# Performance work log

Hardware: AMD Instinct MI355X
Metric: run time of the kernel (lower is better)

## Reference

```python
import jax, jax.numpy as jnp
import numpy as np

B, S, D_MODEL = 2, 4096, 2048
N_IDX_HEADS, D_HEAD = 4, 64


def setup_inputs() -> dict:
    key = jax.random.key(0)
    k1, k2, k3 = jax.random.split(key, 3)
    h = jax.random.normal(k1, (B, S, D_MODEL), dtype=jnp.float32)
    # torch Linear weights: [out_features, in_features]
    Wq = jax.random.normal(k2, (N_IDX_HEADS * D_HEAD, D_MODEL), dtype=jnp.float32) * (D_MODEL ** -0.5)
    Wk = jax.random.normal(k3, (D_HEAD, D_MODEL), dtype=jnp.float32) * (D_MODEL ** -0.5)
    w = jnp.ones((N_IDX_HEADS,), dtype=jnp.float32)
    return {"h": h, "Wq": Wq, "Wk": Wk, "w": w}


def reference(h, Wq, Wk, w):
    batch, seq, _ = h.shape
    # q: [B, T, H, Dh]; k: [B, S, Dh]
    q = (h @ Wq.T).reshape(batch, seq, N_IDX_HEADS, D_HEAD)
    k = h @ Wk.T
    # scores: [B, T, H, S]
    scores = jax.nn.relu(jnp.einsum('bthd,bsd->bths', q, k))
    # head-weighted sum -> I: [B, T, S]
    I = jnp.einsum('bths,h->bts', scores, w)
    return I
```

## Files before the change

kernel.cpp:

```cpp
#include <hip/hip_runtime.h>

typedef __attribute__((ext_vector_type(8))) short bf16x8;
typedef __attribute__((ext_vector_type(4))) float f32x4;
typedef __attribute__((ext_vector_type(8))) unsigned short us8;

#define K_DIM 2048
#define QK_N  320
#define SEQ   4096
#define BK    64
#define NCHUNK 32
#define NHALF  160
#define BCHUNK 20480

__device__ __forceinline__ unsigned short f2bf(float f) {
    unsigned int u = __builtin_bit_cast(unsigned int, f);
    u += 0x7FFFu + ((u >> 16) & 1u);
    return (unsigned short)(u >> 16);
}

__global__ void cvt_w_swz(const float* __restrict__ Wq,
                          const float* __restrict__ Wk,
                          unsigned short* __restrict__ ws) {
    int id = blockIdx.x * 256 + threadIdx.x;
    int c  = id >> 8;
    int k8 = id & 255;
    int k0 = k8 * 8;
    const float* src = (c < 256) ? (Wq + (size_t)c * K_DIM + k0)
                                 : (Wk + (size_t)(c - 256) * K_DIM + k0);
    float4 v0 = *reinterpret_cast<const float4*>(src);
    float4 v1 = *reinterpret_cast<const float4*>(src + 4);
    us8 o;
    o[0] = f2bf(v0.x); o[1] = f2bf(v0.y); o[2] = f2bf(v0.z); o[3] = f2bf(v0.w);
    o[4] = f2bf(v1.x); o[5] = f2bf(v1.y); o[6] = f2bf(v1.z); o[7] = f2bf(v1.w);
    int half = (c >= NHALF) ? 1 : 0;
    int cc   = c - half * NHALF;
    int kc = k0 / BK;
    int u  = (k0 % BK) >> 3;
    size_t byteoff = (size_t)half * (NCHUNK * (size_t)BCHUNK)
                   + (size_t)kc * BCHUNK + ((size_t)(u * NHALF + cc) * 16);
    *reinterpret_cast<us8*>((char*)ws + byteoff) = o;
}

__global__ __launch_bounds__(256) void proj_gemm(
    const float* __restrict__ A,
    const unsigned short* __restrict__ Wsz,
    unsigned short* __restrict__ C)
{
    const int tid  = threadIdx.x;
    const int lane = tid & 63;
    const int wid  = tid >> 6;
    const int rg   = wid >> 1;
    const int cg   = wid & 1;
    const int half = blockIdx.x;
    const int row0 = blockIdx.y * 32 + rg * 16;
    const int lr = lane & 15, lg = lane >> 4;

    const float* ap = A + (size_t)(row0 + lr) * K_DIM + lg * 8;
    const char* wbase = (const char*)Wsz + (size_t)half * (NCHUNK * (size_t)BCHUNK)
                      + ((cg * 80 + lr) << 4);

    f32x4 acc[5];
#pragma unroll
    for (int j = 0; j < 5; ++j) acc[j] = (f32x4)0.f;

#pragma unroll 2
    for (int t = 0; t < 64; ++t) {
        const char* bu = wbase + (size_t)(t >> 1) * BCHUNK
                       + (size_t)(((t & 1) * 4 + lg) * NHALF) * 16;
        bf16x8 b0 = *reinterpret_cast<const bf16x8*>(bu);
        bf16x8 b1 = *reinterpret_cast<const bf16x8*>(bu + 256);
        bf16x8 b2 = *reinterpret_cast<const bf16x8*>(bu + 512);
        bf16x8 b3 = *reinterpret_cast<const bf16x8*>(bu + 768);
        bf16x8 b4 = *reinterpret_cast<const bf16x8*>(bu + 1024);
        const float* p = ap + t * 32;
        float4 x = *reinterpret_cast<const float4*>(p);
        float4 y = *reinterpret_cast<const float4*>(p + 4);
        bf16x8 a;
        a[0] = (short)f2bf(x.x); a[1] = (short)f2bf(x.y);
        a[2] = (short)f2bf(x.z); a[3] = (short)f2bf(x.w);
        a[4] = (short)f2bf(y.x); a[5] = (short)f2bf(y.y);
        a[6] = (short)f2bf(y.z); a[7] = (short)f2bf(y.w);
        acc[0] = __builtin_amdgcn_mfma_f32_16x16x32_bf16(a, b0, acc[0], 0, 0, 0);
        acc[1] = __builtin_amdgcn_mfma_f32_16x16x32_bf16(a, b1, acc[1], 0, 0, 0);
        acc[2] = __builtin_amdgcn_mfma_f32_16x16x32_bf16(a, b2, acc[2], 0, 0, 0);
        acc[3] = __builtin_amdgcn_mfma_f32_16x16x32_bf16(a, b3, acc[3], 0, 0, 0);
        acc[4] = __builtin_amdgcn_mfma_f32_16x16x32_bf16(a, b4, acc[4], 0, 0, 0);
    }

    const int crow = row0 + lg * 4;
    const int ccol = half * NHALF + cg * 80 + lr;
#pragma unroll
    for (int j = 0; j < 5; ++j)
#pragma unroll
        for (int r = 0; r < 4; ++r)
            C[(size_t)(crow + r) * QK_N + ccol + j * 16] = f2bf(acc[j][r]);
}

__global__ __launch_bounds__(256) void scores_kernel(
    const unsigned short* __restrict__ QK,
    const float* __restrict__ w,
    float* __restrict__ out)
{
    const int lane = threadIdx.x & 63;
    const int wid  = threadIdx.x >> 6;
    const int b  = blockIdx.z;
    const int t0 = blockIdx.y * 128 + (wid >> 1) * 64;
    const int s0 = blockIdx.x * 128 + (wid & 1) * 64;

    const int lr = lane & 15;
    const int lk = (lane >> 4) * 8;
    const int lg = lane >> 4;

    const unsigned short* Qb = QK + (size_t)b * SEQ * QK_N;
    const unsigned short* Kb = Qb + 256;

    float wv[4] = { w[0], w[1], w[2], w[3] };

    f32x4 fin[4][4];
#pragma unroll
    for (int i = 0; i < 4; ++i)
#pragma unroll
        for (int j = 0; j < 4; ++j) fin[i][j] = (f32x4)0.f;

    const unsigned short* qp = Qb + (size_t)(t0 + lr) * QK_N + lk;
    const unsigned short* kp = Kb + (size_t)(s0 + lr) * QK_N + lk;

#pragma unroll
    for (int h = 0; h < 4; ++h) {
        f32x4 acc[4][4];
#pragma unroll
        for (int i = 0; i < 4; ++i)
#pragma unroll
            for (int j = 0; j < 4; ++j) acc[i][j] = (f32x4)0.f;

#pragma unroll
        for (int ks = 0; ks < 2; ++ks) {
            bf16x8 qf[4], kf[4];
#pragma unroll
            for (int i = 0; i < 4; ++i)
                qf[i] = *reinterpret_cast<const bf16x8*>(
                    qp + (size_t)i * 16 * QK_N + h * 64 + ks * 32);
#pragma unroll
            for (int j = 0; j < 4; ++j)
                kf[j] = *reinterpret_cast<const bf16x8*>(
                    kp + (size_t)j * 16 * QK_N + ks * 32);
#pragma unroll
            for (int i = 0; i < 4; ++i)
#pragma unroll
                for (int j = 0; j < 4; ++j)
                    acc[i][j] = __builtin_amdgcn_mfma_f32_16x16x32_bf16(kf[j], qf[i], acc[i][j], 0, 0, 0);
        }
#pragma unroll
        for (int i = 0; i < 4; ++i)
#pragma unroll
            for (int j = 0; j < 4; ++j)
#pragma unroll
                for (int r = 0; r < 4; ++r)
                    fin[i][j][r] += wv[h] * fmaxf(acc[i][j][r], 0.f);
    }

    float* ob = out + (size_t)b * SEQ * SEQ;
#pragma unroll
    for (int i = 0; i < 4; ++i) {
        const size_t rbase = (size_t)(t0 + i * 16 + lr) * SEQ + s0 + lg * 4;
#pragma unroll
        for (int j = 0; j < 4; ++j) {
            float4 v;
            v.x = fin[i][j][0]; v.y = fin[i][j][1];
            v.z = fin[i][j][2]; v.w = fin[i][j][3];
            *reinterpret_cast<float4*>(&ob[rbase + j * 16]) = v;
        }
    }
}

extern "C" void kernel_launch(void* const* d_in, const int* in_sizes, int n_in,
                              void* d_out, int out_size, void* d_ws, size_t ws_size,
                              hipStream_t stream) {
    const float* h  = (const float*)d_in[0];
    const float* Wq = (const float*)d_in[1];
    const float* Wk = (const float*)d_in[2];
    const float* w  = (const float*)d_in[3];
    float* out = (float*)d_out;

    unsigned short* W_swz = (unsigned short*)d_ws;
    unsigned short* QKb   = (unsigned short*)((char*)d_ws + 2 * (size_t)NCHUNK * BCHUNK);

    cvt_w_swz<<<320, 256, 0, stream>>>(Wq, Wk, W_swz);
    proj_gemm<<<dim3(2, 256), 256, 0, stream>>>(h, W_swz, QKb);
    scores_kernel<<<dim3(32, 32, 2), 256, 0, stream>>>(QKb, w, out);
}
```

Measured before the change: 124.3 us.

## Split-K projection GEMM with fp32 partials, reduce kernel, and software-pipelined loads

Splits the K dimension of the projection GEMM into two segments, which doubles the number of blocks (2x256x2) so more of the GPU is filled. Each segment writes fp32 partial results to workspace, and a new reduce kernel sums them and converts to bf16. The inner loop is also rewritten with explicit double-buffered register prefetching of the A and B fragments, and launch bounds now request 4 blocks per CU. The cost is extra fp32 partial-buffer traffic (about 21 MB written and read back) plus one more kernel launch.

```diff
diff --git a/kernel.cpp b/kernel.cpp
--- a/kernel.cpp
+++ b/kernel.cpp
@@ -3,6 +3,7 @@
 typedef __attribute__((ext_vector_type(8))) short bf16x8;
 typedef __attribute__((ext_vector_type(4))) float f32x4;
 typedef __attribute__((ext_vector_type(8))) unsigned short us8;
+typedef __attribute__((ext_vector_type(4))) unsigned short us4;
 
 #define K_DIM 2048
 #define QK_N  320
@@ -11,6 +12,9 @@
 #define NCHUNK 32
 #define NHALF  160
 #define BCHUNK 20480
+#define KSPLIT 2
+#define SEGCHUNK (NCHUNK / KSPLIT)
+#define CPART_ELEMS ((size_t)8192 * QK_N)
 
 __device__ __forceinline__ unsigned short f2bf(float f) {
     unsigned int u = __builtin_bit_cast(unsigned int, f);
@@ -41,10 +45,10 @@
     *reinterpret_cast<us8*>((char*)ws + byteoff) = o;
 }
 
-__global__ __launch_bounds__(256) void proj_gemm(
+__global__ __launch_bounds__(256, 4) void proj_gemm(
     const float* __restrict__ A,
     const unsigned short* __restrict__ Wsz,
-    unsigned short* __restrict__ C)
+    float* __restrict__ Cpart)
 {
     const int tid  = threadIdx.x;
     const int lane = tid & 63;
@@ -52,48 +56,84 @@
     const int rg   = wid >> 1;
     const int cg   = wid & 1;
     const int half = blockIdx.x;
+    const int kseg = blockIdx.z;
     const int row0 = blockIdx.y * 32 + rg * 16;
     const int lr = lane & 15, lg = lane >> 4;
 
-    const float* ap = A + (size_t)(row0 + lr) * K_DIM + lg * 8;
+    const float* ap = A + (size_t)(row0 + lr) * K_DIM + kseg * (K_DIM / KSPLIT) + lg * 8;
     const char* wbase = (const char*)Wsz + (size_t)half * (NCHUNK * (size_t)BCHUNK)
+                      + (size_t)(kseg * SEGCHUNK) * BCHUNK
                       + ((cg * 80 + lr) << 4);
 
     f32x4 acc[5];
 #pragma unroll
     for (int j = 0; j < 5; ++j) acc[j] = (f32x4)0.f;
 
-#pragma unroll 2
-    for (int t = 0; t < 64; ++t) {
-        const char* bu = wbase + (size_t)(t >> 1) * BCHUNK
-                       + (size_t)(((t & 1) * 4 + lg) * NHALF) * 16;
-        bf16x8 b0 = *reinterpret_cast<const bf16x8*>(bu);
-        bf16x8 b1 = *reinterpret_cast<const bf16x8*>(bu + 256);
-        bf16x8 b2 = *reinterpret_cast<const bf16x8*>(bu + 512);
-        bf16x8 b3 = *reinterpret_cast<const bf16x8*>(bu + 768);
-        bf16x8 b4 = *reinterpret_cast<const bf16x8*>(bu + 1024);
-        const float* p = ap + t * 32;
-        float4 x = *reinterpret_cast<const float4*>(p);
-        float4 y = *reinterpret_cast<const float4*>(p + 4);
-        bf16x8 a;
-        a[0] = (short)f2bf(x.x); a[1] = (short)f2bf(x.y);
-        a[2] = (short)f2bf(x.z); a[3] = (short)f2bf(x.w);
-        a[4] = (short)f2bf(y.x); a[5] = (short)f2bf(y.y);
-        a[6] = (short)f2bf(y.z); a[7] = (short)f2bf(y.w);
-        acc[0] = __builtin_amdgcn_mfma_f32_16x16x32_bf16(a, b0, acc[0], 0, 0, 0);
-        acc[1] = __builtin_amdgcn_mfma_f32_16x16x32_bf16(a, b1, acc[1], 0, 0, 0);
-        acc[2] = __builtin_amdgcn_mfma_f32_16x16x32_bf16(a, b2, acc[2], 0, 0, 0);
-        acc[3] = __builtin_amdgcn_mfma_f32_16x16x32_bf16(a, b3, acc[3], 0, 0, 0);
-        acc[4] = __builtin_amdgcn_mfma_f32_16x16x32_bf16(a, b4, acc[4], 0, 0, 0);
+#define LOADB(t, b0, b1, b2, b3, b4) do {                                   \
+        const char* bu = wbase + (size_t)((t) >> 1) * BCHUNK                \
+                       + (size_t)((((t) & 1) * 4 + lg) * NHALF) * 16;       \
+        b0 = *reinterpret_cast<const bf16x8*>(bu);                          \
+        b1 = *reinterpret_cast<const bf16x8*>(bu + 256);                    \
+        b2 = *reinterpret_cast<const bf16x8*>(bu + 512);                    \
+        b3 = *reinterpret_cast<const bf16x8*>(bu + 768);                    \
+        b4 = *reinterpret_cast<const bf16x8*>(bu + 1024);                   \
+    } while (0)
+#define LOADA(t, vx, vy) do {                                               \
+        const float* p = ap + (t) * 32;                                     \
+        vx = *reinterpret_cast<const float4*>(p);                           \
+        vy = *reinterpret_cast<const float4*>(p + 4);                       \
+    } while (0)
+#define COMPUTE(vx, vy, b0, b1, b2, b3, b4) do {                            \
+        bf16x8 a_;                                                          \
+        a_[0] = (short)f2bf(vx.x); a_[1] = (short)f2bf(vx.y);               \
+        a_[2] = (short)f2bf(vx.z); a_[3] = (short)f2bf(vx.w);               \
+        a_[4] = (short)f2bf(vy.x); a_[5] = (short)f2bf(vy.y);               \
+        a_[6] = (short)f2bf(vy.z); a_[7] = (short)f2bf(vy.w);               \
+        acc[0] = __builtin_amdgcn_mfma_f32_16x16x32_bf16(a_, b0, acc[0], 0, 0, 0); \
+        acc[1] = __builtin_amdgcn_mfma_f32_16x16x32_bf16(a_, b1, acc[1], 0, 0, 0); \
+        acc[2] = __builtin_amdgcn_mfma_f32_16x16x32_bf16(a_, b2, acc[2], 0, 0, 0); \
+        acc[3] = __builtin_amdgcn_mfma_f32_16x16x32_bf16(a_, b3, acc[3], 0, 0, 0); \
+        acc[4] = __builtin_amdgcn_mfma_f32_16x16x32_bf16(a_, b4, acc[4], 0, 0, 0); \
+    } while (0)
+
+    bf16x8 cb0, cb1, cb2, cb3, cb4;  float4 cvx, cvy;
+    bf16x8 nb0, nb1, nb2, nb3, nb4;  float4 nvx, nvy;
+
+    LOADB(0, cb0, cb1, cb2, cb3, cb4);
+    LOADA(0, cvx, cvy);
+
+    for (int t = 0; t < 32; t += 2) {
+        LOADB(t + 1, nb0, nb1, nb2, nb3, nb4);
+        LOADA(t + 1, nvx, nvy);
+        COMPUTE(cvx, cvy, cb0, cb1, cb2, cb3, cb4);
+        const int t2 = (t + 2 < 32) ? t + 2 : 31;
+        LOADB(t2, cb0, cb1, cb2, cb3, cb4);
+        LOADA(t2, cvx, cvy);
+        COMPUTE(nvx, nvy, nb0, nb1, nb2, nb3, nb4);
     }
-
+#undef LOADB
+#undef LOADA
+#undef COMPUTE
+
+    float* cp = Cpart + (size_t)kseg * CPART_ELEMS;
     const int crow = row0 + lg * 4;
     const int ccol = half * NHALF + cg * 80 + lr;
 #pragma unroll
     for (int j = 0; j < 5; ++j)
 #pragma unroll
         for (int r = 0; r < 4; ++r)
-            C[(size_t)(crow + r) * QK_N + ccol + j * 16] = f2bf(acc[j][r]);
+            cp[(size_t)(crow + r) * QK_N + ccol + j * 16] = acc[j][r];
+}
+
+__global__ void reduce_cvt(const float* __restrict__ Cpart,
+                           unsigned short* __restrict__ QKb) {
+    int i = blockIdx.x * 256 + threadIdx.x;
+    float4 a = reinterpret_cast<const float4*>(Cpart)[i];
+    float4 b = reinterpret_cast<const float4*>(Cpart + CPART_ELEMS)[i];
+    us4 o;
+    o[0] = f2bf(a.x + b.x); o[1] = f2bf(a.y + b.y);
+    o[2] = f2bf(a.z + b.z); o[3] = f2bf(a.w + b.w);
+    reinterpret_cast<us4*>(QKb)[i] = o;
 }
 
 __global__ __launch_bounds__(256) void scores_kernel(
@@ -182,10 +222,15 @@
     const float* w  = (const float*)d_in[3];
     float* out = (float*)d_out;
 
-    unsigned short* W_swz = (unsigned short*)d_ws;
-    unsigned short* QKb   = (unsigned short*)((char*)d_ws + 2 * (size_t)NCHUNK * BCHUNK);
+    char* ws = (char*)d_ws;
+    unsigned short* W_swz = (unsigned short*)ws;
+    ws += 2 * (size_t)NCHUNK * BCHUNK;
+    unsigned short* QKb = (unsigned short*)ws;
+    ws += (size_t)8192 * QK_N * 2;
+    float* Cpart = (float*)ws;
 
     cvt_w_swz<<<320, 256, 0, stream>>>(Wq, Wk, W_swz);
-    proj_gemm<<<dim3(2, 256), 256, 0, stream>>>(h, W_swz, QKb);
+    proj_gemm<<<dim3(2, 256, KSPLIT), 256, 0, stream>>>(h, W_swz, Cpart);
+    reduce_cvt<<<(int)(CPART_ELEMS / 4 / 256), 256, 0, stream>>>(Cpart, QKb);
     scores_kernel<<<dim3(32, 32, 2), 256, 0, stream>>>(QKb, w, out);
 }
```

After: 124.1 us. No clear change (-0.2%).

## Pre-convert activations to swizzled bf16 and software-pipeline projection GEMM loads

Applied to the files above, without the earlier changes.

Adds a separate kernel that converts h to bf16 and writes it in an MFMA-fragment-swizzled layout, so the projection GEMM reads contiguous 16-byte A fragments instead of fp32 rows that it converts in the loop. The GEMM loop is rewritten with explicit double-buffered register prefetch of A and B fragments, and launch bounds now request 2 blocks per CU. In exchange it adds an extra kernel launch and a full read of h plus a write and re-read of a 32 MB bf16 copy.

```diff
diff --git a/kernel.cpp b/kernel.cpp
--- a/kernel.cpp
+++ b/kernel.cpp
@@ -11,6 +11,7 @@
 #define NCHUNK 32
 #define NHALF  160
 #define BCHUNK 20480
+#define STRIP_BYTES 131072
 
 __device__ __forceinline__ unsigned short f2bf(float f) {
     unsigned int u = __builtin_bit_cast(unsigned int, f);
@@ -41,8 +42,33 @@
     *reinterpret_cast<us8*>((char*)ws + byteoff) = o;
 }
 
-__global__ __launch_bounds__(256) void proj_gemm(
-    const float* __restrict__ A,
+__global__ __launch_bounds__(256) void cvt_h_swz(
+    const float* __restrict__ h, char* __restrict__ hs) {
+    const int strip = blockIdx.x >> 2;
+    const int q     = blockIdx.x & 3;
+    char* sbase = hs + (size_t)strip * STRIP_BYTES;
+#pragma unroll
+    for (int i = 0; i < 8; ++i) {
+        int row = q * 8 + i;
+        int k8  = threadIdx.x;
+        const float* src = h + (size_t)(strip * 32 + row) * K_DIM + k8 * 8;
+        float4 v0 = *reinterpret_cast<const float4*>(src);
+        float4 v1 = *reinterpret_cast<const float4*>(src + 4);
+        us8 o;
+        o[0] = f2bf(v0.x); o[1] = f2bf(v0.y); o[2] = f2bf(v0.z); o[3] = f2bf(v0.w);
+        o[4] = f2bf(v1.x); o[5] = f2bf(v1.y); o[6] = f2bf(v1.z); o[7] = f2bf(v1.w);
+        int t  = k8 >> 2;
+        int lg = k8 & 3;
+        int rg = row >> 4;
+        int lr = row & 15;
+        size_t off = (size_t)t * 2048 + (size_t)rg * 1024
+                   + (size_t)(lg * 16 + lr) * 16;
+        *reinterpret_cast<us8*>(sbase + off) = o;
+    }
+}
+
+__global__ __launch_bounds__(256, 2) void proj_gemm(
+    const char* __restrict__ Hs,
     const unsigned short* __restrict__ Wsz,
     unsigned short* __restrict__ C)
 {
@@ -55,7 +81,8 @@
     const int row0 = blockIdx.y * 32 + rg * 16;
     const int lr = lane & 15, lg = lane >> 4;
 
-    const float* ap = A + (size_t)(row0 + lr) * K_DIM + lg * 8;
+    const char* ahp = Hs + (size_t)blockIdx.y * STRIP_BYTES
+                    + (size_t)rg * 1024 + (size_t)lane * 16;
     const char* wbase = (const char*)Wsz + (size_t)half * (NCHUNK * (size_t)BCHUNK)
                       + ((cg * 80 + lr) << 4);
 
@@ -63,29 +90,44 @@
 #pragma unroll
     for (int j = 0; j < 5; ++j) acc[j] = (f32x4)0.f;
 
-#pragma unroll 2
-    for (int t = 0; t < 64; ++t) {
-        const char* bu = wbase + (size_t)(t >> 1) * BCHUNK
-                       + (size_t)(((t & 1) * 4 + lg) * NHALF) * 16;
-        bf16x8 b0 = *reinterpret_cast<const bf16x8*>(bu);
-        bf16x8 b1 = *reinterpret_cast<const bf16x8*>(bu + 256);
-        bf16x8 b2 = *reinterpret_cast<const bf16x8*>(bu + 512);
-        bf16x8 b3 = *reinterpret_cast<const bf16x8*>(bu + 768);
-        bf16x8 b4 = *reinterpret_cast<const bf16x8*>(bu + 1024);
-        const float* p = ap + t * 32;
-        float4 x = *reinterpret_cast<const float4*>(p);
-        float4 y = *reinterpret_cast<const float4*>(p + 4);
-        bf16x8 a;
-        a[0] = (short)f2bf(x.x); a[1] = (short)f2bf(x.y);
-        a[2] = (short)f2bf(x.z); a[3] = (short)f2bf(x.w);
-        a[4] = (short)f2bf(y.x); a[5] = (short)f2bf(y.y);
-        a[6] = (short)f2bf(y.z); a[7] = (short)f2bf(y.w);
-        acc[0] = __builtin_amdgcn_mfma_f32_16x16x32_bf16(a, b0, acc[0], 0, 0, 0);
-        acc[1] = __builtin_amdgcn_mfma_f32_16x16x32_bf16(a, b1, acc[1], 0, 0, 0);
-        acc[2] = __builtin_amdgcn_mfma_f32_16x16x32_bf16(a, b2, acc[2], 0, 0, 0);
-        acc[3] = __builtin_amdgcn_mfma_f32_16x16x32_bf16(a, b3, acc[3], 0, 0, 0);
-        acc[4] = __builtin_amdgcn_mfma_f32_16x16x32_bf16(a, b4, acc[4], 0, 0, 0);
-    }
+#define LOADB(t, b0, b1, b2, b3, b4) do {                                   \
+        const char* bu = wbase + (size_t)((t) >> 1) * BCHUNK                \
+                       + (size_t)((((t) & 1) * 4 + lg) * NHALF) * 16;       \
+        b0 = *reinterpret_cast<const bf16x8*>(bu);                          \
+        b1 = *reinterpret_cast<const bf16x8*>(bu + 256);                    \
+        b2 = *reinterpret_cast<const bf16x8*>(bu + 512);                    \
+        b3 = *reinterpret_cast<const bf16x8*>(bu + 768);                    \
+        b4 = *reinterpret_cast<const bf16x8*>(bu + 1024);                   \
+    } while (0)
+#define LOADA(t, a) do {                                                    \
+        a = *reinterpret_cast<const bf16x8*>(ahp + (size_t)(t) * 2048);     \
+    } while (0)
+#define COMPUTE(a, b0, b1, b2, b3, b4) do {                                 \
+        acc[0] = __builtin_amdgcn_mfma_f32_16x16x32_bf16(a, b0, acc[0], 0, 0, 0); \
+        acc[1] = __builtin_amdgcn_mfma_f32_16x16x32_bf16(a, b1, acc[1], 0, 0, 0); \
+        acc[2] = __builtin_amdgcn_mfma_f32_16x16x32_bf16(a, b2, acc[2], 0, 0, 0); \
+        acc[3] = __builtin_amdgcn_mfma_f32_16x16x32_bf16(a, b3, acc[3], 0, 0, 0); \
+        acc[4] = __builtin_amdgcn_mfma_f32_16x16x32_bf16(a, b4, acc[4], 0, 0, 0); \
+    } while (0)
+
+    bf16x8 cb0, cb1, cb2, cb3, cb4, ca;
+    bf16x8 nb0, nb1, nb2, nb3, nb4, na;
+
+    LOADB(0, cb0, cb1, cb2, cb3, cb4);
+    LOADA(0, ca);
+
+    for (int t = 0; t < 64; t += 2) {
+        LOADB(t + 1, nb0, nb1, nb2, nb3, nb4);
+        LOADA(t + 1, na);
+        COMPUTE(ca, cb0, cb1, cb2, cb3, cb4);
+        const int t2 = (t + 2 < 64) ? t + 2 : 63;
+        LOADB(t2, cb0, cb1, cb2, cb3, cb4);
+        LOADA(t2, ca);
+        COMPUTE(na, nb0, nb1, nb2, nb3, nb4);
+    }
+#undef LOADB
+#undef LOADA
+#undef COMPUTE
 
     const int crow = row0 + lg * 4;
     const int ccol = half * NHALF + cg * 80 + lr;
@@ -182,10 +224,15 @@
     const float* w  = (const float*)d_in[3];
     float* out = (float*)d_out;
 
-    unsigned short* W_swz = (unsigned short*)d_ws;
-    unsigned short* QKb   = (unsigned short*)((char*)d_ws + 2 * (size_t)NCHUNK * BCHUNK);
+    char* ws = (char*)d_ws;
+    unsigned short* W_swz = (unsigned short*)ws;
+    ws += 2 * (size_t)NCHUNK * BCHUNK;
+    char* H_swz = ws;
+    ws += (size_t)256 * STRIP_BYTES;
+    unsigned short* QKb = (unsigned short*)ws;
 
     cvt_w_swz<<<320, 256, 0, stream>>>(Wq, Wk, W_swz);
-    proj_gemm<<<dim3(2, 256), 256, 0, stream>>>(h, W_swz, QKb);
+    cvt_h_swz<<<1024, 256, 0, stream>>>(h, H_swz);
+    proj_gemm<<<dim3(2, 256), 256, 0, stream>>>(H_swz, W_swz, QKb);
     scores_kernel<<<dim3(32, 32, 2), 256, 0, stream>>>(QKb, w, out);
 }
```

Result: slower. 154.4 us (+24.2%).
